# Kernel tuning notes

Measured on AMD Instinct MI355X. Metric: run time of the kernel, lower is better.

Reference implementation:

```python
import jax, jax.numpy as jnp
import numpy as np

N_NODES = 50000
N_EDGES = 800000
D_IN = 96
D_HID = 96
D_OUT = 4


def _glorot(key, shape):
    lim = float(np.sqrt(6.0 / (shape[0] + shape[1])))
    return jax.random.uniform(key, shape, jnp.float32, -lim, lim)


def setup_inputs() -> dict:
    key = jax.random.key(0)
    ks = jax.random.split(key, 8)
    x = jax.random.normal(ks[0], (N_NODES, D_IN), jnp.float32)
    edge_index = jax.random.randint(ks[1], (2, N_EDGES), 0, N_NODES, jnp.int64)
    return {
        'x': x,
        'edge_index': edge_index,
        'W0': _glorot(ks[2], (D_IN, D_HID)), 'b0': jnp.zeros((D_HID,), jnp.float32),
        'W1': _glorot(ks[3], (D_HID, D_HID)), 'b1': jnp.zeros((D_HID,), jnp.float32),
        'W2': _glorot(ks[4], (D_HID, D_HID)), 'b2': jnp.zeros((D_HID,), jnp.float32),
        'Wfc': _glorot(ks[5], (D_HID, D_OUT)), 'bfc': jnp.zeros((D_OUT,), jnp.float32),
    }


def _gcn_conv(x, src, dst, W, b, n):
    # GCNConv: linear transform, add self-loops, symmetric degree norm, scatter-add.
    h = x @ W                                   # [N, D]
    loops = jnp.arange(n, dtype=src.dtype)
    s = jnp.concatenate([src, loops])           # [E+N]
    d = jnp.concatenate([dst, loops])
    deg = jax.ops.segment_sum(jnp.ones_like(d, dtype=h.dtype), d, num_segments=n)
    dinv = jnp.where(deg > 0, jax.lax.rsqrt(deg), 0.0)
    norm = dinv[s] * dinv[d]                    # [E+N]
    msgs = h[s] * norm[:, None]                 # gather + scale
    out = jax.ops.segment_sum(msgs, d, num_segments=n)  # scatter-add
    return out + b


def reference(x, edge_index, W0, b0, W1, b1, W2, b2, Wfc, bfc):
    src, dst = edge_index[0], edge_index[1]
    n = x.shape[0]
    h = jax.nn.relu(_gcn_conv(x, src, dst, W0, b0, n))   # dropout = identity (eval)
    h = jax.nn.relu(_gcn_conv(h, src, dst, W1, b1, n))
    h = jax.nn.relu(_gcn_conv(h, src, dst, W2, b2, n))
    return h @ Wfc + bfc
```

## Files before the change

### kernel.cpp

```cpp
#include <hip/hip_runtime.h>

typedef __bf16 bf16x8 __attribute__((ext_vector_type(8)));
typedef float  f32x4  __attribute__((ext_vector_type(4)));
typedef float  f32x8  __attribute__((ext_vector_type(8)));
typedef unsigned short ushort;
typedef ushort us8 __attribute__((ext_vector_type(8)));

constexpr int N_NODES = 50000;
constexpr int N_EDGES = 800000;
constexpr int SLOTS = 64;
constexpr int GE   = N_EDGES / 256;
constexpr int WBLK = (3 * 9216) / 256;
constexpr int GMF  = (N_NODES + 63) / 64;

__device__ inline float h16f(ushort u) {
    union { _Float16 h; ushort u; } cv; cv.u = u; return (float)cv.h;
}
__device__ inline ushort f16b(float f) {
    union { _Float16 h; ushort u; } cv; cv.h = (_Float16)f; return cv.u;
}
__device__ inline ushort bf16b(float f) {
    union { __bf16 b; ushort u; } cv; cv.b = (__bf16)f; return cv.u;
}
__device__ inline f32x8 bf8_to_f32(us8 u) {
    f32x8 r;
#pragma unroll
    for (int i = 0; i < 8; ++i) r[i] = __uint_as_float(((unsigned int)u[i]) << 16);
    return r;
}

__global__ __launch_bounds__(256) void k_count(const int* __restrict__ dst,
                                               int* __restrict__ cnt,
                                               ushort* __restrict__ rank,
                                               const float* __restrict__ W0,
                                               const float* __restrict__ W1,
                                               const float* __restrict__ W2,
                                               ushort* __restrict__ Wt) {
    const int b = blockIdx.x;
    if (b < GE) {
        int e = b * 256 + threadIdx.x;
        rank[e] = (ushort)atomicAdd(&cnt[dst[e]], 1);
    } else {
        int i = (b - GE) * 256 + threadIdx.x;
        int m = i / 9216, li = i - m * 9216;
        const float* W = (m == 0) ? W0 : (m == 1) ? W1 : W2;
        int k = li / 96, c = li - k * 96;
        Wt[m * 9216 + c * 96 + k] = bf16b(W[li]);
    }
}

__device__ __forceinline__ void mfma_store(const ushort* sX, const ushort* sW,
                                           ushort* __restrict__ Y, int rowbase) {
    const int tid = threadIdx.x;
    const int wv = tid >> 6, lane = tid & 63, quad = lane >> 4, l16 = lane & 15;
    f32x4 acc[6];
#pragma unroll
    for (int t = 0; t < 6; ++t) acc[t] = (f32x4){0.f, 0.f, 0.f, 0.f};

    const ushort* ax = sX + (wv * 16 + l16) * 96 + quad * 8;
#pragma unroll
    for (int s = 0; s < 3; ++s) {
        bf16x8 a = *(const bf16x8*)(ax + s * 32);
#pragma unroll
        for (int t = 0; t < 6; ++t) {
            bf16x8 b = *(const bf16x8*)(sW + (t * 16 + l16) * 96 + s * 32 + quad * 8);
            acc[t] = __builtin_amdgcn_mfma_f32_16x16x32_bf16(a, b, acc[t], 0, 0, 0);
        }
    }
    const int r0 = rowbase + wv * 16 + quad * 4;
#pragma unroll
    for (int t = 0; t < 6; ++t) {
#pragma unroll
        for (int g = 0; g < 4; ++g) {
            int r = r0 + g;
            if (r < N_NODES) Y[(size_t)r * 96 + t * 16 + l16] = bf16b(acc[t][g]);
        }
    }
}

__global__ __launch_bounds__(256) void k_fill_gemm1(const int* __restrict__ src,
                                                    const int* __restrict__ dst,
                                                    const int* __restrict__ cnt,
                                                    const ushort* __restrict__ rank,
                                                    unsigned int* __restrict__ csr,
                                                    const float* __restrict__ x,
                                                    const ushort* __restrict__ Wt,
                                                    ushort* __restrict__ H) {
    __shared__ ushort sS[64 * 96 + 96 * 96];
    const int b = blockIdx.x;
    const int tid = threadIdx.x;
    if (b < GE) {
        int e = b * 256 + tid;
        int s = src[e], d = dst[e];
        float hs = rsqrtf((float)(cnt[s] + 1));
        unsigned int entry = (unsigned int)(ushort)s | ((unsigned int)f16b(hs) << 16);
        csr[(size_t)d * SLOTS + rank[e]] = entry;
    } else {
        ushort* sX = sS;
        ushort* sW = sS + 64 * 96;
        const int rowbase = (b - GE) * 64;
        for (int i = tid; i < 9216 / 8; i += 256)
            ((uint4*)sW)[i] = ((const uint4*)Wt)[i];
        for (int i = tid; i < 64 * 24; i += 256) {
            int r = i / 24, c4 = i % 24;
            int gr = rowbase + r;
            float4 v = make_float4(0.f, 0.f, 0.f, 0.f);
            if (gr < N_NODES) v = ((const float4*)(x + (size_t)gr * 96))[c4];
            ushort* p = sX + r * 96 + c4 * 4;
            p[0] = bf16b(v.x); p[1] = bf16b(v.y); p[2] = bf16b(v.z); p[3] = bf16b(v.w);
        }
        __syncthreads();
        mfma_store(sX, sW, H, rowbase);
    }
}

__global__ __launch_bounds__(256) void k_gemm_b(const ushort* __restrict__ X,
                                                const ushort* __restrict__ Wt,
                                                ushort* __restrict__ Y) {
    __shared__ ushort sS[64 * 96 + 96 * 96];
    ushort* sX = sS;
    ushort* sW = sS + 64 * 96;
    const int tid = threadIdx.x;
    const int rowbase = blockIdx.x * 64;
    for (int i = tid; i < 9216 / 8; i += 256)
        ((uint4*)sW)[i] = ((const uint4*)Wt)[i];
    for (int i = tid; i < 64 * 12; i += 256) {
        int r = i / 12, c8 = i % 12;
        int gr = rowbase + r;
        uint4 v = make_uint4(0, 0, 0, 0);
        if (gr < N_NODES) v = ((const uint4*)(X + (size_t)gr * 96))[c8];
        ((uint4*)(sX + r * 96))[c8] = v;
    }
    __syncthreads();
    mfma_store(sX, sW, Y, rowbase);
}

template<int MODE>
__global__ __launch_bounds__(192) void k_agg(const ushort* __restrict__ A,
                                             const int* __restrict__ cnt,
                                             const unsigned int* __restrict__ csr,
                                             const float* __restrict__ bias,
                                             ushort* __restrict__ Hout,
                                             float* __restrict__ out4,
                                             const float* __restrict__ Wfc,
                                             const float* __restrict__ bfc) {
    __shared__ float sWfc[384];
    __shared__ float red[16][12][4];
    const int tid = threadIdx.x;
    if (MODE == 1) {
        for (int i = tid; i < 384; i += 192) sWfc[i] = Wfc[i];
        __syncthreads();
    }
    const int g = tid / 12, c = tid % 12;
    const int n = blockIdx.x * 16 + g;

    const int deg = cnt[n];
    const float dn = rsqrtf((float)(deg + 1));
    us8 a0 = *(const us8*)(A + (size_t)n * 96 + c * 8);
    f32x8 acc = bf8_to_f32(a0) * (dn * dn);

    const unsigned int* row = csr + (size_t)n * SLOTS;
    int j = 0;
    for (; j + 8 <= deg; j += 8) {
        const uint4 q0 = *(const uint4*)(row + j);
        const uint4 q1 = *(const uint4*)(row + j + 4);
        const us8 u0 = *(const us8*)(A + (size_t)(q0.x & 0xFFFFu) * 96 + c * 8);
        const us8 u1 = *(const us8*)(A + (size_t)(q0.y & 0xFFFFu) * 96 + c * 8);
        const us8 u2 = *(const us8*)(A + (size_t)(q0.z & 0xFFFFu) * 96 + c * 8);
        const us8 u3 = *(const us8*)(A + (size_t)(q0.w & 0xFFFFu) * 96 + c * 8);
        const us8 u4 = *(const us8*)(A + (size_t)(q1.x & 0xFFFFu) * 96 + c * 8);
        const us8 u5 = *(const us8*)(A + (size_t)(q1.y & 0xFFFFu) * 96 + c * 8);
        const us8 u6 = *(const us8*)(A + (size_t)(q1.z & 0xFFFFu) * 96 + c * 8);
        const us8 u7 = *(const us8*)(A + (size_t)(q1.w & 0xFFFFu) * 96 + c * 8);
        acc += bf8_to_f32(u0) * (h16f((ushort)(q0.x >> 16)) * dn);
        acc += bf8_to_f32(u1) * (h16f((ushort)(q0.y >> 16)) * dn);
        acc += bf8_to_f32(u2) * (h16f((ushort)(q0.z >> 16)) * dn);
        acc += bf8_to_f32(u3) * (h16f((ushort)(q0.w >> 16)) * dn);
        acc += bf8_to_f32(u4) * (h16f((ushort)(q1.x >> 16)) * dn);
        acc += bf8_to_f32(u5) * (h16f((ushort)(q1.y >> 16)) * dn);
        acc += bf8_to_f32(u6) * (h16f((ushort)(q1.z >> 16)) * dn);
        acc += bf8_to_f32(u7) * (h16f((ushort)(q1.w >> 16)) * dn);
    }
    for (; j + 4 <= deg; j += 4) {
        const uint4 q = *(const uint4*)(row + j);
        const us8 u0 = *(const us8*)(A + (size_t)(q.x & 0xFFFFu) * 96 + c * 8);
        const us8 u1 = *(const us8*)(A + (size_t)(q.y & 0xFFFFu) * 96 + c * 8);
        const us8 u2 = *(const us8*)(A + (size_t)(q.z & 0xFFFFu) * 96 + c * 8);
        const us8 u3 = *(const us8*)(A + (size_t)(q.w & 0xFFFFu) * 96 + c * 8);
        acc += bf8_to_f32(u0) * (h16f((ushort)(q.x >> 16)) * dn);
        acc += bf8_to_f32(u1) * (h16f((ushort)(q.y >> 16)) * dn);
        acc += bf8_to_f32(u2) * (h16f((ushort)(q.z >> 16)) * dn);
        acc += bf8_to_f32(u3) * (h16f((ushort)(q.w >> 16)) * dn);
    }
    for (; j < deg; ++j) {
        const unsigned int e = row[j];
        const float w = h16f((ushort)(e >> 16)) * dn;
        const us8 u = *(const us8*)(A + (size_t)(e & 0xFFFFu) * 96 + c * 8);
        acc += bf8_to_f32(u) * w;
    }
#pragma unroll
    for (int f = 0; f < 8; ++f) acc[f] = fmaxf(acc[f] + bias[c * 8 + f], 0.0f);

    if (MODE == 0) {
        us8 o;
#pragma unroll
        for (int f = 0; f < 8; ++f) o[f] = bf16b(acc[f]);
        *(us8*)(Hout + (size_t)n * 96 + c * 8) = o;
    } else {
        float p0 = 0.f, p1 = 0.f, p2 = 0.f, p3 = 0.f;
#pragma unroll
        for (int f = 0; f < 8; ++f) {
            const float* wr = sWfc + (c * 8 + f) * 4;
            p0 += acc[f] * wr[0];
            p1 += acc[f] * wr[1];
            p2 += acc[f] * wr[2];
            p3 += acc[f] * wr[3];
        }
        red[g][c][0] = p0; red[g][c][1] = p1; red[g][c][2] = p2; red[g][c][3] = p3;
        __syncthreads();
        if (tid < 64) {
            const int gg = tid >> 2, jj = tid & 3;
            float s = bfc[jj];
#pragma unroll
            for (int cc = 0; cc < 12; ++cc) s += red[gg][cc][jj];
            out4[(size_t)(blockIdx.x * 16 + gg) * 4 + jj] = s;
        }
    }
}

extern "C" void kernel_launch(void* const* d_in, const int* in_sizes, int n_in,
                              void* d_out, int out_size, void* d_ws, size_t ws_size,
                              hipStream_t stream) {
    const float* x   = (const float*)d_in[0];
    const int*   ei  = (const int*)d_in[1];
    const int*   src = ei;
    const int*   dst = ei + N_EDGES;
    const float* W0  = (const float*)d_in[2];
    const float* b0  = (const float*)d_in[3];
    const float* W1  = (const float*)d_in[4];
    const float* b1  = (const float*)d_in[5];
    const float* W2  = (const float*)d_in[6];
    const float* b2  = (const float*)d_in[7];
    const float* Wfc = (const float*)d_in[8];
    const float* bfc = (const float*)d_in[9];
    float* out = (float*)d_out;

    char* w = (char*)d_ws;
    unsigned int* csr = (unsigned int*)w;  w += ((size_t)N_NODES * SLOTS * 4 + 15) & ~15ULL;
    int*    cnt  = (int*)w;                w += ((size_t)N_NODES * 4 + 15) & ~15ULL;
    ushort* rank = (ushort*)w;             w += ((size_t)N_EDGES * 2 + 15) & ~15ULL;
    ushort* Wt   = (ushort*)w;             w += ((size_t)3 * 9216 * 2 + 15) & ~15ULL;
    ushort* H    = (ushort*)w;             w += ((size_t)N_NODES * 96 * 2 + 15) & ~15ULL;
    ushort* G    = (ushort*)w;

    const int gAgg = N_NODES / 16;

    (void)hipMemsetAsync(cnt, 0, (size_t)N_NODES * 4, stream);
    hipLaunchKernelGGL(k_count, dim3(GE + WBLK), dim3(256), 0, stream,
                       dst, cnt, rank, W0, W1, W2, Wt);
    hipLaunchKernelGGL(k_fill_gemm1, dim3(GE + GMF), dim3(256), 0, stream,
                       src, dst, cnt, rank, csr, x, Wt, H);
    hipLaunchKernelGGL((k_agg<0>), dim3(gAgg), dim3(192), 0, stream,
                       H, cnt, csr, b0, G, (float*)nullptr,
                       (const float*)nullptr, (const float*)nullptr);
    hipLaunchKernelGGL(k_gemm_b, dim3(GMF), dim3(256), 0, stream, G, Wt + 9216, H);
    hipLaunchKernelGGL((k_agg<0>), dim3(gAgg), dim3(192), 0, stream,
                       H, cnt, csr, b1, G, (float*)nullptr,
                       (const float*)nullptr, (const float*)nullptr);
    hipLaunchKernelGGL(k_gemm_b, dim3(GMF), dim3(256), 0, stream, G, Wt + 2 * 9216, H);
    hipLaunchKernelGGL((k_agg<1>), dim3(gAgg), dim3(192), 0, stream,
                       H, cnt, csr, b2, (ushort*)nullptr, out, Wfc, bfc);
}
```

Before: 236.0 us.

## Fuse neighbor aggregation with the following layer GEMM in one kernel

Replaces the separate aggregation and GEMM kernels for layers 1 and 2 with a single kernel. Each 768-thread block first aggregates 64 nodes into shared memory as bf16 with bias and ReLU, then multiplies them by the next layer's weights using MFMA. This removes two launches and the round trip of the intermediate activations through global memory. In exchange it uses large blocks with fewer nodes per block, which may hurt gather latency hiding and occupancy. The aggregated activations also pass through a bf16 conversion.

```diff
diff --git a/kernel.cpp b/kernel.cpp
--- a/kernel.cpp
+++ b/kernel.cpp
@@ -114,25 +114,108 @@
     }
 }
 
-__global__ __launch_bounds__(256) void k_gemm_b(const ushort* __restrict__ X,
-                                                const ushort* __restrict__ Wt,
-                                                ushort* __restrict__ Y) {
+__global__ __launch_bounds__(768) void k_agg_gemm(const ushort* __restrict__ A,
+                                                  const int* __restrict__ cnt,
+                                                  const unsigned int* __restrict__ csr,
+                                                  const float* __restrict__ bias,
+                                                  const ushort* __restrict__ Wt,
+                                                  ushort* __restrict__ Y) {
     __shared__ ushort sS[64 * 96 + 96 * 96];
     ushort* sX = sS;
     ushort* sW = sS + 64 * 96;
     const int tid = threadIdx.x;
     const int rowbase = blockIdx.x * 64;
-    for (int i = tid; i < 9216 / 8; i += 256)
+
+    for (int i = tid; i < 9216 / 8; i += 768)
         ((uint4*)sW)[i] = ((const uint4*)Wt)[i];
-    for (int i = tid; i < 64 * 12; i += 256) {
-        int r = i / 12, c8 = i % 12;
-        int gr = rowbase + r;
-        uint4 v = make_uint4(0, 0, 0, 0);
-        if (gr < N_NODES) v = ((const uint4*)(X + (size_t)gr * 96))[c8];
-        ((uint4*)(sX + r * 96))[c8] = v;
+
+    const int g = tid / 12;
+    const int c = tid - g * 12;
+    const int n = rowbase + g;
+
+    f32x8 acc = (f32x8){0.f, 0.f, 0.f, 0.f, 0.f, 0.f, 0.f, 0.f};
+    if (n < N_NODES) {
+        const int deg = cnt[n];
+        const float dn = rsqrtf((float)(deg + 1));
+        us8 a0 = *(const us8*)(A + (size_t)n * 96 + c * 8);
+        acc = bf8_to_f32(a0) * (dn * dn);
+
+        const unsigned int* row = csr + (size_t)n * SLOTS;
+        int j = 0;
+        for (; j + 8 <= deg; j += 8) {
+            const uint4 q0 = *(const uint4*)(row + j);
+            const uint4 q1 = *(const uint4*)(row + j + 4);
+            const us8 u0 = *(const us8*)(A + (size_t)(q0.x & 0xFFFFu) * 96 + c * 8);
+            const us8 u1 = *(const us8*)(A + (size_t)(q0.y & 0xFFFFu) * 96 + c * 8);
+            const us8 u2 = *(const us8*)(A + (size_t)(q0.z & 0xFFFFu) * 96 + c * 8);
+            const us8 u3 = *(const us8*)(A + (size_t)(q0.w & 0xFFFFu) * 96 + c * 8);
+            const us8 u4 = *(const us8*)(A + (size_t)(q1.x & 0xFFFFu) * 96 + c * 8);
+            const us8 u5 = *(const us8*)(A + (size_t)(q1.y & 0xFFFFu) * 96 + c * 8);
+            const us8 u6 = *(const us8*)(A + (size_t)(q1.z & 0xFFFFu) * 96 + c * 8);
+            const us8 u7 = *(const us8*)(A + (size_t)(q1.w & 0xFFFFu) * 96 + c * 8);
+            acc += bf8_to_f32(u0) * (h16f((ushort)(q0.x >> 16)) * dn);
+            acc += bf8_to_f32(u1) * (h16f((ushort)(q0.y >> 16)) * dn);
+            acc += bf8_to_f32(u2) * (h16f((ushort)(q0.z >> 16)) * dn);
+            acc += bf8_to_f32(u3) * (h16f((ushort)(q0.w >> 16)) * dn);
+            acc += bf8_to_f32(u4) * (h16f((ushort)(q1.x >> 16)) * dn);
+            acc += bf8_to_f32(u5) * (h16f((ushort)(q1.y >> 16)) * dn);
+            acc += bf8_to_f32(u6) * (h16f((ushort)(q1.z >> 16)) * dn);
+            acc += bf8_to_f32(u7) * (h16f((ushort)(q1.w >> 16)) * dn);
+        }
+        for (; j + 4 <= deg; j += 4) {
+            const uint4 q = *(const uint4*)(row + j);
+            const us8 u0 = *(const us8*)(A + (size_t)(q.x & 0xFFFFu) * 96 + c * 8);
+            const us8 u1 = *(const us8*)(A + (size_t)(q.y & 0xFFFFu) * 96 + c * 8);
+            const us8 u2 = *(const us8*)(A + (size_t)(q.z & 0xFFFFu) * 96 + c * 8);
+            const us8 u3 = *(const us8*)(A + (size_t)(q.w & 0xFFFFu) * 96 + c * 8);
+            acc += bf8_to_f32(u0) * (h16f((ushort)(q.x >> 16)) * dn);
+            acc += bf8_to_f32(u1) * (h16f((ushort)(q.y >> 16)) * dn);
+            acc += bf8_to_f32(u2) * (h16f((ushort)(q.z >> 16)) * dn);
+            acc += bf8_to_f32(u3) * (h16f((ushort)(q.w >> 16)) * dn);
+        }
+        for (; j < deg; ++j) {
+            const unsigned int e = row[j];
+            const float w = h16f((ushort)(e >> 16)) * dn;
+            const us8 u = *(const us8*)(A + (size_t)(e & 0xFFFFu) * 96 + c * 8);
+            acc += bf8_to_f32(u) * w;
+        }
+#pragma unroll
+        for (int f = 0; f < 8; ++f) acc[f] = fmaxf(acc[f] + bias[c * 8 + f], 0.0f);
+    }
+    {
+        us8 o;
+#pragma unroll
+        for (int f = 0; f < 8; ++f) o[f] = bf16b(acc[f]);
+        *(us8*)(sX + g * 96 + c * 8) = o;
     }
     __syncthreads();
-    mfma_store(sX, sW, Y, rowbase);
+
+    const int wv = tid >> 6;
+    const int lane = tid & 63, quad = lane >> 4, l16 = lane & 15;
+    const int t0 = 2 * wv;
+    const int rg = t0 / 6;
+    const int ct0 = t0 - rg * 6;
+
+    f32x4 acc0 = (f32x4){0.f, 0.f, 0.f, 0.f};
+    f32x4 acc1 = (f32x4){0.f, 0.f, 0.f, 0.f};
+    const ushort* ax = sX + (rg * 16 + l16) * 96 + quad * 8;
+#pragma unroll
+    for (int s = 0; s < 3; ++s) {
+        bf16x8 a = *(const bf16x8*)(ax + s * 32);
+        bf16x8 b0 = *(const bf16x8*)(sW + (ct0 * 16 + l16) * 96 + s * 32 + quad * 8);
+        bf16x8 b1 = *(const bf16x8*)(sW + ((ct0 + 1) * 16 + l16) * 96 + s * 32 + quad * 8);
+        acc0 = __builtin_amdgcn_mfma_f32_16x16x32_bf16(a, b0, acc0, 0, 0, 0);
+        acc1 = __builtin_amdgcn_mfma_f32_16x16x32_bf16(a, b1, acc1, 0, 0, 0);
+    }
+    const int r0 = rowbase + rg * 16 + quad * 4;
+#pragma unroll
+    for (int gg = 0; gg < 4; ++gg) {
+        int r = r0 + gg;
+        if (r < N_NODES) {
+            Y[(size_t)r * 96 + ct0 * 16 + l16]       = bf16b(acc0[gg]);
+            Y[(size_t)r * 96 + (ct0 + 1) * 16 + l16] = bf16b(acc1[gg]);
+        }
+    }
 }
 
 template<int MODE>
@@ -260,14 +343,10 @@
                        dst, cnt, rank, W0, W1, W2, Wt);
     hipLaunchKernelGGL(k_fill_gemm1, dim3(GE + GMF), dim3(256), 0, stream,
                        src, dst, cnt, rank, csr, x, Wt, H);
-    hipLaunchKernelGGL((k_agg<0>), dim3(gAgg), dim3(192), 0, stream,
-                       H, cnt, csr, b0, G, (float*)nullptr,
-                       (const float*)nullptr, (const float*)nullptr);
-    hipLaunchKernelGGL(k_gemm_b, dim3(GMF), dim3(256), 0, stream, G, Wt + 9216, H);
-    hipLaunchKernelGGL((k_agg<0>), dim3(gAgg), dim3(192), 0, stream,
-                       H, cnt, csr, b1, G, (float*)nullptr,
-                       (const float*)nullptr, (const float*)nullptr);
-    hipLaunchKernelGGL(k_gemm_b, dim3(GMF), dim3(256), 0, stream, G, Wt + 2 * 9216, H);
+    hipLaunchKernelGGL(k_agg_gemm, dim3(GMF), dim3(768), 0, stream,
+                       H, cnt, csr, b0, Wt + 9216, G);
+    hipLaunchKernelGGL(k_agg_gemm, dim3(GMF), dim3(768), 0, stream,
+                       G, cnt, csr, b1, Wt + 2 * 9216, H);
     hipLaunchKernelGGL((k_agg<1>), dim3(gAgg), dim3(192), 0, stream,
                        H, cnt, csr, b2, (ushort*)nullptr, out, Wfc, bfc);
 }
```

New measurement: 224.5 us. -4.8%, faster.
